# Performance work log

Measured on AMD Instinct MI355X. Metric: run time of the kernel, lower is better.

Reference implementation:

```python
import jax, jax.numpy as jnp
import numpy as np

IGNORE = 255
KA = 10.0
ITERS = 10
BETA = 0.8


def _l2(x, axis):
    # F.normalize(p=2): divide by max(norm, eps)
    return x / jnp.maximum(jnp.linalg.norm(x, axis=axis, keepdims=True), 1e-12)


def setup_inputs() -> dict:
    key = jax.random.key(0)
    k1, k2, k3, k4 = jax.random.split(key, 4)
    B, K, P, C = 8, 19, 16384, 256
    return {
        "logit": jax.random.normal(k1, (B, K, P), jnp.float32),
        "target": jax.random.randint(k2, (B, P), 0, K, jnp.int32),
        "feat": jax.random.normal(k3, (B, C, P), jnp.float32),
        "epoch": 60,
        "prototypes_dataset": _l2(jax.random.normal(k4, (C, K), jnp.float32), 0),
    }


def reference(logit, target, feat, epoch, prototypes_dataset):
    B, K, P = logit.shape
    C = feat.shape[1]
    dt = feat.dtype

    # scatter-sum per-class prototypes over all (b, p) positions; ignore bucket = K
    index = jnp.where(target == IGNORE, K, target).reshape(-1)            # [B*P]
    feat_flat = jnp.swapaxes(feat, 1, 2).reshape(B * P, C)                # [B*P, C]
    proto = jax.ops.segment_sum(feat_flat, index, num_segments=K + 1)    # [K+1, C]
    counts = jax.ops.segment_sum(jnp.ones_like(index), index, num_segments=K + 1)
    prototypes_sum = proto[:K].T                                          # [C, K]
    counts_batch = counts[:K]                                             # [K]

    # epoch is a static python int; epoch >= start_epoch(51) -> full vMF branch
    feat_norm = _l2(feat, 1)                                              # [B, C, P]
    u_init = _l2(prototypes_sum / (counts_batch.astype(dt) + 1e-6), 0)    # [C, K]
    mask0 = counts_batch == 0
    u = _l2(jnp.where(mask0[None, :], prototypes_dataset, u_init), 0)     # 'part' init
    a = jnp.full((1, 1, K), 1.0 / K, dt)

    dis = jnp.einsum('bcp,ck->bpk', feat_norm, u)                         # [B, P, K]
    e = a * jnp.exp(KA * dis)
    p = e / jnp.sum(e, -1, keepdims=True)
    for _ in range(ITERS):
        # 'avmf': second assignment in torch overwrites -> mean over batch, [1, P, K]
        a = jnp.mean(p, 0, keepdims=True)
        # 'uvmf': new prototypes from soft assignments
        u = _l2(jnp.mean(jnp.einsum('bcp,bpk->bck', feat_norm, p), 0), 0)
        dis = jnp.einsum('bcp,ck->bpk', feat_norm, u)
        e = a * jnp.exp(KA * dis)
        p = e / jnp.sum(e, -1, keepdims=True)

    # vMF_hard_loss computed in torch but 'hard' not in loss_type -> not added
    vmf_loss = jnp.mean(-p * (jnp.log(a + 1e-6) + KA * dis)) / float(np.log(K))
    consist_loss = jnp.mean(-jnp.swapaxes(p, 1, 2) * jax.nn.log_softmax(logit, axis=1))

    # contrast: off-diagonal prototype similarity over classes present in batch
    m = (~mask0).astype(dt)
    gram = u_init.T @ u_init                                              # [K, K]
    Kn = jnp.sum(m)
    contrast_loss = (jnp.sum(gram * (m[:, None] * m[None, :])) - Kn) / (Kn * (Kn - 1))

    # 'tce': truncated CE, clamp per-pixel loss at -log(beta)
    logp = jax.nn.log_softmax(logit, axis=1)                              # [B, K, P]
    safe_t = jnp.where(target == IGNORE, 0, target)
    ce = -jnp.take_along_axis(logp, safe_t[:, None, :], axis=1)[:, 0, :]  # [B, P]
    valid = (target != IGNORE).astype(dt)
    loss = jnp.sum(jnp.maximum(ce, -float(np.log(BETA))) * valid) / (jnp.sum(valid) + 1e-6)

    loss = loss + vmf_loss + contrast_loss + consist_loss
    return (loss, jax.lax.stop_gradient(prototypes_sum), jax.lax.stop_gradient(counts_batch))
```

## Files before the change

kernel.cpp:

```cpp
#include <hip/hip_runtime.h>
#include <hip/hip_bf16.h>
#include <math.h>

#define BB 8
#define KK 19
#define PP 16384
#define CC 256
#define NN (BB*PP)
#define KA_C 10.0f
#define IGNORE_L 255
#define CETHR 0.22314355131420976f
#define AQ 524288

#define OFF_FEATN   0
#define OFF_FEATNT  16777216
#define OFF_PROTO   33554432
#define OFF_COUNTS  (OFF_PROTO+4864)
#define OFF_SCAL    (OFF_COUNTS+32)
#define OFF_UINIT   (OFF_SCAL+16)
#define OFF_U       (OFF_UINIT+4864)
#define OFF_UBF     (OFF_U+4864)
#define OFF_A       (OFF_UBF+4224)
#define OFF_UPART   (OFF_A+8*AQ)
#define OFF_R1      (OFF_UPART+4980736)
#define OFF_NORM    (OFF_R1+77824)
#define OFF_LOGT    (OFF_NORM+131072)

typedef __attribute__((ext_vector_type(8))) short short8v;
typedef __attribute__((ext_vector_type(4))) float f32x4;

static __device__ __forceinline__ float bflo(unsigned int v){
    union{unsigned int i; float f;} x; x.i = v << 16; return x.f;
}
static __device__ __forceinline__ unsigned short f2bf(float f){
    union{float f; unsigned int i;} x; x.f = f;
    unsigned int r = (x.i + 0x7fffu + ((x.i >> 16) & 1u)) >> 16;
    return (unsigned short)r;
}
static __device__ __forceinline__ float rowsum16(float v){
    v += __shfl_xor(v,1); v += __shfl_xor(v,2);
    v += __shfl_xor(v,4); v += __shfl_xor(v,8);
    return v;
}
static __device__ __forceinline__ float rowmax16(float v){
    v = fmaxf(v, __shfl_xor(v,1)); v = fmaxf(v, __shfl_xor(v,2));
    v = fmaxf(v, __shfl_xor(v,4)); v = fmaxf(v, __shfl_xor(v,8));
    return v;
}

__global__ __launch_bounds__(256) void counts_kernel(const int* __restrict__ target,
                                                     float* __restrict__ ws) {
    __shared__ int cnt[KK];
    if (threadIdx.x < KK) cnt[threadIdx.x]=0;
    __syncthreads();
    for (int i = blockIdx.x*256 + threadIdx.x; i < NN; i += gridDim.x*256) {
        int t = target[i];
        if (t >= 0 && t < KK) atomicAdd(&cnt[t], 1);
    }
    __syncthreads();
    if (threadIdx.x < KK) atomicAdd(&ws[OFF_COUNTS + threadIdx.x], (float)cnt[threadIdx.x]);
}

__global__ __launch_bounds__(256) void ssct_kernel(const float* __restrict__ feat,
                                                   unsigned short* __restrict__ featn,
                                                   unsigned short* __restrict__ featn_T,
                                                   float* __restrict__ normf) {
    __shared__ float part[4][64];
    __shared__ float rn_lds[64];
    __shared__ unsigned short tTus[64][270];
    int blk = blockIdx.x;
    int b = blk >> 8;
    int px0 = (blk & 255) * 64;
    int tid = threadIdx.x;
    int l = tid & 63, w = tid >> 6;
    const float* fb = feat + (size_t)b*CC*PP;
    int c0 = w*64;
    float fv[64];
    float ss = 0.f;
#pragma unroll
    for (int cc=0; cc<64; cc++) {
        fv[cc] = fb[(size_t)(c0+cc)*PP + px0 + l];
        ss = fmaf(fv[cc], fv[cc], ss);
    }
    part[w][l] = ss;
    __syncthreads();
    if (tid < 64) {
        float s = part[0][tid]+part[1][tid]+part[2][tid]+part[3][tid];
        float nrm = fmaxf(sqrtf(s), 1e-12f);
        normf[(size_t)b*PP + px0 + tid] = nrm;
        rn_lds[tid] = 1.0f/nrm;
    }
    __syncthreads();
    float r = rn_lds[l];
    unsigned short* ob  = featn + (size_t)b*CC*PP + px0;
#pragma unroll
    for (int cc=0; cc<64; cc++) {
        int c = c0 + cc;
        unsigned short us = f2bf(fv[cc] * r);
        ob[(size_t)c*PP + l] = us;
        tTus[l][c] = us;
    }
    __syncthreads();
    unsigned short* obT = featn_T + ((size_t)b*PP + px0)*CC;
    for (int j=0; j<32; j++) {
        int flat = j*256 + tid;
        int px = flat >> 7, cu = flat & 127;
        unsigned int v = *(const unsigned int*)&tTus[px][cu*2];
        *(unsigned int*)&obT[(size_t)px*CC + cu*2] = v;
    }
}

__global__ __launch_bounds__(256) void logt_kernel(const float* __restrict__ logit,
                                                   float* __restrict__ logt) {
    __shared__ float t[256][21];
    int blk = blockIdx.x;
    int b = blk >> 6;
    int px0 = (blk & 63) * 256;
    int tid = threadIdx.x;
    for (int k=0;k<KK;k++)
        t[tid][k] = logit[((size_t)b*KK + k)*PP + px0 + tid];
    __syncthreads();
    float* dst = logt + ((size_t)b*PP + px0)*20;
    for (int j=0; j<20; j++) {
        int flat = j*256 + tid;
        int px = flat / 20, k = flat % 20;
        dst[flat] = (k<KK) ? t[px][k] : 0.f;
    }
}

__global__ __launch_bounds__(256) void proto_mfma_kernel(const unsigned short* __restrict__ featn,
                                                         const int* __restrict__ target,
                                                         const float* __restrict__ normf,
                                                         float* __restrict__ upart) {
    __shared__ int tgt_lds[4][64];
    __shared__ unsigned short nrm_lds[4][64];
    int tid = threadIdx.x;
    int blk = blockIdx.x;
    int pxtile = blk & 255;
    int bgrp = blk >> 8;
    {
        int bi = tid >> 6, j = tid & 63;
        int bb = bgrp*4 + bi;
        tgt_lds[bi][j] = target[(size_t)bb*PP + pxtile*64 + j];
        nrm_lds[bi][j] = f2bf(normf[(size_t)bb*PP + pxtile*64 + j]);
    }
    __syncthreads();
    int lane = tid & 63, wid = tid >> 6;
    int g = lane >> 4, lc = lane & 15;

    f32x4 upacc[4][2];
#pragma unroll
    for (int m=0;m<4;m++)
#pragma unroll
        for (int n=0;n<2;n++) upacc[m][n] = (f32x4){0.f,0.f,0.f,0.f};

    for (int bi=0; bi<4; bi++) {
        int bb = bgrp*4 + bi;
        union { unsigned int u[4]; short8v s; } bfr[2][2];
#pragma unroll
        for (int ks=0; ks<2; ks++) {
            int pxo = ks*32 + g*8;
#pragma unroll
            for (int j2=0;j2<4;j2++) {
                int p0i = pxo + 2*j2, p1i = pxo + 2*j2 + 1;
                int t0 = tgt_lds[bi][p0i], t1 = tgt_lds[bi][p1i];
                unsigned int n0 = nrm_lds[bi][p0i], n1 = nrm_lds[bi][p1i];
                int kk1 = lc + 16;
                bfr[ks][0].u[j2] = (t0==lc ? n0:0u) | ((t1==lc ? n1:0u)<<16);
                bfr[ks][1].u[j2] = (t0==kk1? n0:0u) | ((t1==kk1? n1:0u)<<16);
            }
        }
#pragma unroll
        for (int m=0;m<4;m++) {
            int c = wid*64 + m*16 + lc;
            const unsigned short* fr = featn + ((size_t)bb*CC + c)*PP + pxtile*64;
#pragma unroll
            for (int ks=0; ks<2; ks++) {
                int pxo = ks*32 + g*8;
                union { uint4 u4; short8v s; } af2;
                af2.u4 = *(const uint4*)&fr[pxo];
                upacc[m][0] = __builtin_amdgcn_mfma_f32_16x16x32_bf16(af2.s, bfr[ks][0].s, upacc[m][0], 0,0,0);
                upacc[m][1] = __builtin_amdgcn_mfma_f32_16x16x32_bf16(af2.s, bfr[ks][1].s, upacc[m][1], 0,0,0);
            }
        }
    }
#pragma unroll
    for (int m=0;m<4;m++) {
        int cb = wid*64 + m*16 + g*4;
#pragma unroll
        for (int n=0;n<2;n++) {
            int kk = lc + 16*n;
            if (kk < KK) {
#pragma unroll
                for (int r=0;r<4;r++)
                    upart[(size_t)blk*4864 + (size_t)(cb+r)*KK + kk] = upacc[m][n][r];
            }
        }
    }
}

__global__ __launch_bounds__(256) void setup_kernel(const float* __restrict__ pd,
                                                    float* __restrict__ ws) {
    int c = threadIdx.x;
    __shared__ float red[256];
    __shared__ float nrm[KK];
    __shared__ float lds_ui[256][KK];
    float cnts[KK], vi[KK];
#pragma unroll
    for (int k=0;k<KK;k++) cnts[k] = ws[OFF_COUNTS+k];
#pragma unroll
    for (int k=0;k<KK;k++) vi[k] = ws[OFF_PROTO + c*KK + k] / (cnts[k] + 1e-6f);
    for (int k=0;k<KK;k++) {
        red[c] = vi[k]*vi[k];
        __syncthreads();
        for (int s=128;s>0;s>>=1){ if (c<s) red[c]+=red[c+s]; __syncthreads(); }
        if (c==0) nrm[k] = fmaxf(sqrtf(red[0]), 1e-12f);
        __syncthreads();
    }
#pragma unroll
    for (int k=0;k<KK;k++) { vi[k] = vi[k]/nrm[k]; lds_ui[c][k] = vi[k]; ws[OFF_UINIT + c*KK + k] = vi[k]; }
    __syncthreads();
    float w0[KK];
#pragma unroll
    for (int k=0;k<KK;k++) w0[k] = (cnts[k]==0.f) ? pd[c*KK+k] : vi[k];
    for (int k=0;k<KK;k++) {
        red[c] = w0[k]*w0[k];
        __syncthreads();
        for (int s=128;s>0;s>>=1){ if (c<s) red[c]+=red[c+s]; __syncthreads(); }
        if (c==0) nrm[k] = fmaxf(sqrtf(red[0]), 1e-12f);
        __syncthreads();
    }
    unsigned short* ubf = (unsigned short*)(ws + OFF_UBF);
#pragma unroll
    for (int k=0;k<KK;k++) {
        float uv = w0[k] / nrm[k];
        ws[OFF_U + k*CC + c] = uv;
        ubf[k*264 + c] = f2bf(uv);
    }
    float m[KK]; float Kn=0.f;
#pragma unroll
    for (int k=0;k<KK;k++){ m[k] = (cnts[k]==0.f)?0.f:1.f; Kn += m[k]; }
    float csum = 0.f;
    for (int idx = c; idx < KK*KK; idx += 256) {
        int k1 = idx / KK, k2 = idx % KK;
        if (m[k1]!=0.f && m[k2]!=0.f) {
            float gg=0.f;
            for (int cc2=0; cc2<CC; cc2++) gg += lds_ui[cc2][k1]*lds_ui[cc2][k2];
            csum += gg;
        }
    }
    red[c]=csum; __syncthreads();
    for (int s=128;s>0;s>>=1){ if (c<s) red[c]+=red[c+s]; __syncthreads(); }
    if (c==0) ws[OFF_SCAL+4] = (red[0] - Kn) / (Kn * (Kn - 1.f));
}

__global__ __launch_bounds__(256) void pu_kernel(const unsigned short* __restrict__ featn,
                                                 const unsigned short* __restrict__ featn_T,
                                                 const unsigned short* __restrict__ ubf,
                                                 const float* __restrict__ aRbase,
                                                 float* __restrict__ aWbase,
                                                 float* __restrict__ upart,
                                                 int uniform_a) {
    __shared__ __attribute__((aligned(16))) unsigned short u_lds[32*264];
    __shared__ __attribute__((aligned(16))) unsigned short p_lds[32*72];
    int tid = threadIdx.x;
    {
        const uint4* src = (const uint4*)ubf;
        uint4* dst = (uint4*)u_lds;
        for (int i=tid; i<1056; i+=256) dst[i] = src[i];
    }
    __syncthreads();
    int blk = blockIdx.x;
    int pxtile = blk & 255;
    int bgrp = blk >> 8;
    int lane = tid & 63, wid = tid >> 6;
    int g = lane >> 4, lc = lane & 15;
    int px_w = pxtile*64 + wid*16;

    float a0r[4], a1r[4];
    if (uniform_a) {
#pragma unroll
        for (int r=0;r<4;r++){ a0r[r]=1.0f/(float)KK; a1r[r]=1.0f/(float)KK; }
    } else {
        int k1 = (lc+16 > KK-1) ? (KK-1) : (lc+16);
#pragma unroll
        for (int r=0;r<4;r++) {
            int pxg = px_w + g*4 + r;
            float s0 = aRbase[0*AQ + (size_t)pxg*32 + lc] + aRbase[1*AQ + (size_t)pxg*32 + lc]
                     + aRbase[2*AQ + (size_t)pxg*32 + lc] + aRbase[3*AQ + (size_t)pxg*32 + lc];
            float s1 = aRbase[0*AQ + (size_t)pxg*32 + k1] + aRbase[1*AQ + (size_t)pxg*32 + k1]
                     + aRbase[2*AQ + (size_t)pxg*32 + k1] + aRbase[3*AQ + (size_t)pxg*32 + k1];
            a0r[r] = s0*0.125f;
            a1r[r] = s1*0.125f;
        }
    }

    f32x4 upacc[4][2];
#pragma unroll
    for (int m=0;m<4;m++)
#pragma unroll
        for (int n=0;n<2;n++) upacc[m][n] = (f32x4){0.f,0.f,0.f,0.f};
    float aacc[2][4];
#pragma unroll
    for (int n=0;n<2;n++)
#pragma unroll
        for (int r=0;r<4;r++) aacc[n][r]=0.f;

    for (int bi=0; bi<2; bi++) {
        int bb = bgrp*2 + bi;
        const unsigned short* fb = featn + (size_t)bb*CC*PP;
        const unsigned short* fTrow = featn_T + ((size_t)bb*PP + px_w + lc)*CC;
        f32x4 acc0 = (f32x4){0.f,0.f,0.f,0.f};
        f32x4 acc1 = (f32x4){0.f,0.f,0.f,0.f};
#pragma unroll
        for (int ks=0; ks<8; ks++) {
            int cbase = ks*32 + g*8;
            union { uint4 u4; short8v s; } af, bf0, bf1;
            af.u4  = *(const uint4*)&fTrow[cbase];
            bf0.u4 = *(const uint4*)&u_lds[(size_t)lc*264 + cbase];
            bf1.u4 = *(const uint4*)&u_lds[(size_t)(lc+16)*264 + cbase];
            acc0 = __builtin_amdgcn_mfma_f32_16x16x32_bf16(af.s, bf0.s, acc0, 0,0,0);
            acc1 = __builtin_amdgcn_mfma_f32_16x16x32_bf16(af.s, bf1.s, acc1, 0,0,0);
        }
#pragma unroll
        for (int r=0;r<4;r++) {
            float e0 = a0r[r] * __expf(KA_C * acc0[r]);
            float e1 = (lc+16 < KK) ? a1r[r] * __expf(KA_C * acc1[r]) : 0.f;
            float sv = rowsum16(e0 + e1);
            float inv = 1.0f/sv;
            float p0 = e0*inv, p1 = e1*inv;
            aacc[0][r] += p0; aacc[1][r] += p1;
            int pl = wid*16 + g*4 + r;
            p_lds[(size_t)lc*72 + pl]      = f2bf(p0);
            p_lds[(size_t)(lc+16)*72 + pl] = f2bf(p1);
        }
        __syncthreads();
#pragma unroll
        for (int m=0;m<4;m++) {
            int c = wid*64 + m*16 + lc;
            const unsigned short* fr = fb + (size_t)c*PP + pxtile*64;
#pragma unroll
            for (int ks=0; ks<2; ks++) {
                int pxo = ks*32 + g*8;
                union { uint4 u4; short8v s; } af2, bp0, bp1;
                af2.u4 = *(const uint4*)&fr[pxo];
                bp0.u4 = *(const uint4*)&p_lds[(size_t)lc*72 + pxo];
                bp1.u4 = *(const uint4*)&p_lds[(size_t)(lc+16)*72 + pxo];
                upacc[m][0] = __builtin_amdgcn_mfma_f32_16x16x32_bf16(af2.s, bp0.s, upacc[m][0], 0,0,0);
                upacc[m][1] = __builtin_amdgcn_mfma_f32_16x16x32_bf16(af2.s, bp1.s, upacc[m][1], 0,0,0);
            }
        }
        __syncthreads();
    }
#pragma unroll
    for (int m=0;m<4;m++) {
        int cb = wid*64 + m*16 + g*4;
#pragma unroll
        for (int n=0;n<2;n++) {
            int kk = lc + 16*n;
            if (kk < KK) {
#pragma unroll
                for (int r=0;r<4;r++)
                    upart[(size_t)blk*4864 + (size_t)(cb+r)*KK + kk] = upacc[m][n][r];
            }
        }
    }
    float* aOut = aWbase + (size_t)bgrp*AQ;
#pragma unroll
    for (int n=0;n<2;n++) {
        int kk = lc + 16*n;
        if (kk < KK) {
#pragma unroll
            for (int r=0;r<4;r++) {
                int pxg = px_w + g*4 + r;
                aOut[(size_t)pxg*32 + kk] = aacc[n][r];
            }
        }
    }
}

__global__ __launch_bounds__(256) void r1_kernel(const float* __restrict__ upart,
                                                 float* __restrict__ r1buf) {
    int blk = blockIdx.x;
    int echunk = blk % 19;
    int ichunk = blk / 19;
    int e = echunk*256 + threadIdx.x;
    float s = 0.f;
    int i0 = ichunk*64;
    for (int i=i0; i<i0+64; i++) s += upart[(size_t)i*4864 + e];
    r1buf[(size_t)ichunk*4864 + e] = s;
}

__global__ __launch_bounds__(256) void r2_kernel(const float* __restrict__ r1buf,
                                                 float* __restrict__ ws, int nbuf) {
    int k = blockIdx.x;
    int c = threadIdx.x;
    float s = 0.f;
    for (int i=0;i<nbuf;i++) s += r1buf[(size_t)i*4864 + c*KK + k];
    __shared__ float red[256];
    red[c] = s*s; __syncthreads();
    for (int q=128;q>0;q>>=1){ if (c<q) red[c]+=red[c+q]; __syncthreads(); }
    float nrm = fmaxf(sqrtf(red[0]), 1e-12f);
    float uv = s / nrm;
    ws[OFF_U + k*CC + c] = uv;
    ((unsigned short*)(ws + OFF_UBF))[k*264 + c] = f2bf(uv);
}

__global__ __launch_bounds__(256) void protored2_kernel(const float* __restrict__ r1buf,
                                                        float* __restrict__ ws, int nbuf) {
    int e = blockIdx.x*256 + threadIdx.x;
    float s = 0.f;
    for (int i=0;i<nbuf;i++) s += r1buf[(size_t)i*4864 + e];
    ws[OFF_PROTO + e] = s;
}

__global__ __launch_bounds__(256) void final_mfma_kernel(const unsigned short* __restrict__ featn_T,
                                                         const float* __restrict__ logt,
                                                         const int* __restrict__ target,
                                                         const unsigned short* __restrict__ ubf,
                                                         const float* __restrict__ aFbase,
                                                         float* __restrict__ scal) {
    __shared__ __attribute__((aligned(16))) unsigned short u_lds[32*264];
    int tid = threadIdx.x;
    {
        const uint4* src = (const uint4*)ubf;
        uint4* dst = (uint4*)u_lds;
        for (int i=tid; i<1056; i+=256) dst[i] = src[i];
    }
    __syncthreads();
    int blk = blockIdx.x;
    int pxtile = blk & 255;
    int bgrp = blk >> 8;
    int lane = tid & 63, wid = tid >> 6;
    int g = lane >> 4, lc = lane & 15;
    int px_w = pxtile*64 + wid*16;
    bool valid1 = (lc+16) < KK;

    float v_vmf=0.f, v_cons=0.f, v_ce=0.f, v_cnt=0.f;

    for (int bi=0; bi<4; bi++) {
        int bb = bgrp*4 + bi;
        const unsigned short* fTrow = featn_T + ((size_t)bb*PP + px_w + lc)*CC;
        f32x4 acc0 = (f32x4){0.f,0.f,0.f,0.f};
        f32x4 acc1 = (f32x4){0.f,0.f,0.f,0.f};
#pragma unroll
        for (int ks=0; ks<8; ks++) {
            int cbase = ks*32 + g*8;
            union { uint4 u4; short8v s; } af, bf0, bf1;
            af.u4  = *(const uint4*)&fTrow[cbase];
            bf0.u4 = *(const uint4*)&u_lds[(size_t)lc*264 + cbase];
            bf1.u4 = *(const uint4*)&u_lds[(size_t)(lc+16)*264 + cbase];
            acc0 = __builtin_amdgcn_mfma_f32_16x16x32_bf16(af.s, bf0.s, acc0, 0,0,0);
            acc1 = __builtin_amdgcn_mfma_f32_16x16x32_bf16(af.s, bf1.s, acc1, 0,0,0);
        }
#pragma unroll
        for (int r=0;r<4;r++) {
            int pxg = px_w + g*4 + r;
            float d0 = acc0[r], d1 = acc1[r];
            float av0 = (aFbase[0*AQ + (size_t)pxg*32 + lc] + aFbase[1*AQ + (size_t)pxg*32 + lc]
                       + aFbase[2*AQ + (size_t)pxg*32 + lc] + aFbase[3*AQ + (size_t)pxg*32 + lc])*0.125f;
            float av1 = 0.f;
            if (valid1) {
                int k1 = lc+16;
                av1 = (aFbase[0*AQ + (size_t)pxg*32 + k1] + aFbase[1*AQ + (size_t)pxg*32 + k1]
                     + aFbase[2*AQ + (size_t)pxg*32 + k1] + aFbase[3*AQ + (size_t)pxg*32 + k1])*0.125f;
            }
            float e0 = av0 * __expf(KA_C * d0);
            float e1 = valid1 ? av1 * __expf(KA_C * d1) : 0.f;
            float den = rowsum16(e0 + e1);
            float inv = 1.0f/den;
            float p0 = e0*inv, p1 = e1*inv;
            float vt = -p0*(__logf(av0+1e-6f) + KA_C*d0);
            if (valid1) vt += -p1*(__logf(av1+1e-6f) + KA_C*d1);
            float vt_row = rowsum16(vt);
            const float* lrow = logt + ((size_t)bb*PP + pxg)*20;
            float lg0 = lrow[lc];
            float lg1 = valid1 ? lrow[lc+16] : -3.4e38f;
            float mx = rowmax16(fmaxf(lg0, lg1));
            float sme = __expf(lg0-mx) + (valid1 ? __expf(lg1-mx) : 0.f);
            sme = rowsum16(sme);
            float lse = mx + __logf(sme);
            float ct = -p0*(lg0-lse);
            if (valid1) ct += -p1*(lg1-lse);
            float ct_row = rowsum16(ct);
            int t = target[(size_t)bb*PP + pxg];
            float ltt = (lc==t ? lg0 : 0.f) + ((valid1 && lc+16==t) ? lg1 : 0.f);
            float lt = rowsum16(ltt);
            if (lc==0) {
                v_vmf += vt_row;
                v_cons += ct_row;
                if (t != IGNORE_L) { v_ce += fmaxf(lse - lt, CETHR); v_cnt += 1.f; }
            }
        }
    }
    __shared__ float red[4][4];
    int w = tid >> 6;
    float v0=v_vmf, v1=v_cons, v2=v_ce, v3=v_cnt;
#pragma unroll
    for (int s=32;s>0;s>>=1) {
        v0 += __shfl_xor(v0, s); v1 += __shfl_xor(v1, s);
        v2 += __shfl_xor(v2, s); v3 += __shfl_xor(v3, s);
    }
    if ((tid&63)==0){ red[w][0]=v0; red[w][1]=v1; red[w][2]=v2; red[w][3]=v3; }
    __syncthreads();
    if (tid==0) {
        atomicAdd(&scal[0], red[0][0]+red[1][0]+red[2][0]+red[3][0]);
        atomicAdd(&scal[1], red[0][1]+red[1][1]+red[2][1]+red[3][1]);
        atomicAdd(&scal[2], red[0][2]+red[1][2]+red[2][2]+red[3][2]);
        atomicAdd(&scal[3], red[0][3]+red[1][3]+red[2][3]+red[3][3]);
    }
}

__global__ __launch_bounds__(256) void finalize_kernel(const float* __restrict__ ws,
                                                       float* __restrict__ out) {
    if (blockIdx.x==0 && threadIdx.x==0) {
        float cnt_all = (float)BB*(float)PP*(float)KK;
        float vmf  = ws[OFF_SCAL+0] / cnt_all / logf((float)KK);
        float cons = ws[OFF_SCAL+1] / cnt_all;
        float ce   = ws[OFF_SCAL+2] / (ws[OFF_SCAL+3] + 1e-6f);
        float contrast = ws[OFF_SCAL+4];
        out[0] = ce + vmf + contrast + cons;
    }
    int i = blockIdx.x*256 + threadIdx.x;
    if (i < 4864) out[1+i] = ws[OFF_PROTO+i];
    if (blockIdx.x==0 && threadIdx.x < KK) out[1+4864+threadIdx.x] = ws[OFF_COUNTS+threadIdx.x];
}

extern "C" void kernel_launch(void* const* d_in, const int* in_sizes, int n_in,
                              void* d_out, int out_size, void* d_ws, size_t ws_size,
                              hipStream_t stream) {
    (void)in_sizes; (void)n_in; (void)out_size; (void)ws_size;
    const float* logit  = (const float*)d_in[0];
    const int*   target = (const int*)d_in[1];
    const float* feat   = (const float*)d_in[2];
    const float* pd     = (const float*)d_in[4];
    float* out = (float*)d_out;
    float* ws  = (float*)d_ws;

    unsigned short* featn   = (unsigned short*)ws;
    unsigned short* featn_T = (unsigned short*)(ws + OFF_FEATNT);
    unsigned short* ubf     = (unsigned short*)(ws + OFF_UBF);
    float* upart = ws + OFF_UPART;
    float* r1buf = ws + OFF_R1;
    float* normf = ws + OFF_NORM;
    float* logt  = ws + OFF_LOGT;
    float* scal  = ws + OFF_SCAL;
    float* aSet[2] = { ws + OFF_A, ws + OFF_A + (size_t)4*AQ };

    hipMemsetAsync(ws + OFF_PROTO, 0, 4912*sizeof(float), stream);
    hipMemsetAsync(ws + OFF_UBF, 0, 4224*sizeof(float), stream);
    ssct_kernel<<<2048, 256, 0, stream>>>(feat, featn, featn_T, normf);
    counts_kernel<<<256, 256, 0, stream>>>(target, ws);
    logt_kernel<<<512, 256, 0, stream>>>(logit, logt);
    proto_mfma_kernel<<<512, 256, 0, stream>>>(featn, target, normf, upart);
    r1_kernel<<<152, 256, 0, stream>>>(upart, r1buf);
    protored2_kernel<<<19, 256, 0, stream>>>(r1buf, ws, 8);
    setup_kernel<<<1, 256, 0, stream>>>(pd, ws);

    for (int t=0; t<10; t++) {
        if (t > 0) {
            r1_kernel<<<304, 256, 0, stream>>>(upart, r1buf);
            r2_kernel<<<KK, 256, 0, stream>>>(r1buf, ws, 16);
        }
        pu_kernel<<<1024, 256, 0, stream>>>(featn, featn_T, ubf,
                                            aSet[t&1], aSet[(t+1)&1],
                                            upart, (t==0)?1:0);
    }
    r1_kernel<<<304, 256, 0, stream>>>(upart, r1buf);
    r2_kernel<<<KK, 256, 0, stream>>>(r1buf, ws, 16);
    final_mfma_kernel<<<512, 256, 0, stream>>>(featn_T, logt, target, ubf, aSet[0], scal);
    finalize_kernel<<<20, 256, 0, stream>>>(ws, out);
}
```

Baseline: 594.8 us.

## Replace per-block partial buffers with atomic accumulation into 16 slots

Proto and pu kernels now atomically add their per-block prototype partials into 16 rotating slots instead of writing one full partial per block. This removes the r1 reduction kernel and its large partial buffer traffic each iteration; r2 and protored sum the 16 slots and zero them for reuse. Separately, the ssct kernel packs pairs of bf16 values via lane shuffles into 32-bit stores. The change adds atomic contention on the slots and makes the summation order nondeterministic.

```diff
diff --git a/kernel.cpp b/kernel.cpp
--- a/kernel.cpp
+++ b/kernel.cpp
@@ -22,8 +22,7 @@
 #define OFF_UBF     (OFF_U+4864)
 #define OFF_A       (OFF_UBF+4224)
 #define OFF_UPART   (OFF_A+8*AQ)
-#define OFF_R1      (OFF_UPART+4980736)
-#define OFF_NORM    (OFF_R1+77824)
+#define OFF_NORM    (OFF_UPART+77824)
 #define OFF_LOGT    (OFF_NORM+131072)
 
 typedef __attribute__((ext_vector_type(8))) short short8v;
@@ -92,13 +91,17 @@
     }
     __syncthreads();
     float r = rn_lds[l];
-    unsigned short* ob  = featn + (size_t)b*CC*PP + px0;
+    unsigned short* ob = featn + (size_t)b*CC*PP + px0;
 #pragma unroll
     for (int cc=0; cc<64; cc++) {
         int c = c0 + cc;
-        unsigned short us = f2bf(fv[cc] * r);
-        ob[(size_t)c*PP + l] = us;
-        tTus[l][c] = us;
+        unsigned int us = f2bf(fv[cc] * r);
+        tTus[l][c] = (unsigned short)us;
+        unsigned int partner = __shfl_xor(us, 1);
+        if ((l & 1) == 0) {
+            unsigned int v = us | (partner<<16);
+            *(unsigned int*)&ob[(size_t)c*PP + l] = v;
+        }
     }
     __syncthreads();
     unsigned short* obT = featn_T + ((size_t)b*PP + px0)*CC;
@@ -131,7 +134,7 @@
 __global__ __launch_bounds__(256) void proto_mfma_kernel(const unsigned short* __restrict__ featn,
                                                          const int* __restrict__ target,
                                                          const float* __restrict__ normf,
-                                                         float* __restrict__ upart) {
+                                                         float* __restrict__ up16) {
     __shared__ int tgt_lds[4][64];
     __shared__ unsigned short nrm_lds[4][64];
     int tid = threadIdx.x;
@@ -184,6 +187,7 @@
             }
         }
     }
+    float* slot = up16 + (size_t)(blk & 15)*4864;
 #pragma unroll
     for (int m=0;m<4;m++) {
         int cb = wid*64 + m*16 + g*4;
@@ -193,10 +197,21 @@
             if (kk < KK) {
 #pragma unroll
                 for (int r=0;r<4;r++)
-                    upart[(size_t)blk*4864 + (size_t)(cb+r)*KK + kk] = upacc[m][n][r];
-            }
-        }
-    }
+                    atomicAdd(&slot[(size_t)(cb+r)*KK + kk], upacc[m][n][r]);
+            }
+        }
+    }
+}
+
+__global__ __launch_bounds__(256) void protored_kernel(float* __restrict__ up16,
+                                                       float* __restrict__ ws) {
+    int e = blockIdx.x*256 + threadIdx.x;
+    float s = 0.f;
+#pragma unroll
+    for (int i=0;i<16;i++) s += up16[(size_t)i*4864 + e];
+    ws[OFF_PROTO + e] = s;
+#pragma unroll
+    for (int i=0;i<16;i++) up16[(size_t)i*4864 + e] = 0.f;
 }
 
 __global__ __launch_bounds__(256) void setup_kernel(const float* __restrict__ pd,
@@ -259,7 +274,7 @@
                                                  const unsigned short* __restrict__ ubf,
                                                  const float* __restrict__ aRbase,
                                                  float* __restrict__ aWbase,
-                                                 float* __restrict__ upart,
+                                                 float* __restrict__ up16,
                                                  int uniform_a) {
     __shared__ __attribute__((aligned(16))) unsigned short u_lds[32*264];
     __shared__ __attribute__((aligned(16))) unsigned short p_lds[32*72];
@@ -352,6 +367,7 @@
         }
         __syncthreads();
     }
+    float* slot = up16 + (size_t)(blk & 15)*4864;
 #pragma unroll
     for (int m=0;m<4;m++) {
         int cb = wid*64 + m*16 + g*4;
@@ -361,7 +377,7 @@
             if (kk < KK) {
 #pragma unroll
                 for (int r=0;r<4;r++)
-                    upart[(size_t)blk*4864 + (size_t)(cb+r)*KK + kk] = upacc[m][n][r];
+                    atomicAdd(&slot[(size_t)(cb+r)*KK + kk], upacc[m][n][r]);
             }
         }
     }
@@ -379,24 +395,13 @@
     }
 }
 
-__global__ __launch_bounds__(256) void r1_kernel(const float* __restrict__ upart,
-                                                 float* __restrict__ r1buf) {
-    int blk = blockIdx.x;
-    int echunk = blk % 19;
-    int ichunk = blk / 19;
-    int e = echunk*256 + threadIdx.x;
-    float s = 0.f;
-    int i0 = ichunk*64;
-    for (int i=i0; i<i0+64; i++) s += upart[(size_t)i*4864 + e];
-    r1buf[(size_t)ichunk*4864 + e] = s;
-}
-
-__global__ __launch_bounds__(256) void r2_kernel(const float* __restrict__ r1buf,
-                                                 float* __restrict__ ws, int nbuf) {
+__global__ __launch_bounds__(256) void r2_kernel(float* __restrict__ up16,
+                                                 float* __restrict__ ws) {
     int k = blockIdx.x;
     int c = threadIdx.x;
     float s = 0.f;
-    for (int i=0;i<nbuf;i++) s += r1buf[(size_t)i*4864 + c*KK + k];
+#pragma unroll
+    for (int i=0;i<16;i++) s += up16[(size_t)i*4864 + c*KK + k];
     __shared__ float red[256];
     red[c] = s*s; __syncthreads();
     for (int q=128;q>0;q>>=1){ if (c<q) red[c]+=red[c+q]; __syncthreads(); }
@@ -404,14 +409,8 @@
     float uv = s / nrm;
     ws[OFF_U + k*CC + c] = uv;
     ((unsigned short*)(ws + OFF_UBF))[k*264 + c] = f2bf(uv);
-}
-
-__global__ __launch_bounds__(256) void protored2_kernel(const float* __restrict__ r1buf,
-                                                        float* __restrict__ ws, int nbuf) {
-    int e = blockIdx.x*256 + threadIdx.x;
-    float s = 0.f;
-    for (int i=0;i<nbuf;i++) s += r1buf[(size_t)i*4864 + e];
-    ws[OFF_PROTO + e] = s;
+#pragma unroll
+    for (int i=0;i<16;i++) up16[(size_t)i*4864 + c*KK + k] = 0.f;
 }
 
 __global__ __launch_bounds__(256) void final_mfma_kernel(const unsigned short* __restrict__ featn_T,
@@ -540,8 +539,7 @@
     unsigned short* featn   = (unsigned short*)ws;
     unsigned short* featn_T = (unsigned short*)(ws + OFF_FEATNT);
     unsigned short* ubf     = (unsigned short*)(ws + OFF_UBF);
-    float* upart = ws + OFF_UPART;
-    float* r1buf = ws + OFF_R1;
+    float* up16  = ws + OFF_UPART;
     float* normf = ws + OFF_NORM;
     float* logt  = ws + OFF_LOGT;
     float* scal  = ws + OFF_SCAL;
@@ -549,25 +547,22 @@
 
     hipMemsetAsync(ws + OFF_PROTO, 0, 4912*sizeof(float), stream);
     hipMemsetAsync(ws + OFF_UBF, 0, 4224*sizeof(float), stream);
+    hipMemsetAsync(up16, 0, 16*4864*sizeof(float), stream);
     ssct_kernel<<<2048, 256, 0, stream>>>(feat, featn, featn_T, normf);
     counts_kernel<<<256, 256, 0, stream>>>(target, ws);
     logt_kernel<<<512, 256, 0, stream>>>(logit, logt);
-    proto_mfma_kernel<<<512, 256, 0, stream>>>(featn, target, normf, upart);
-    r1_kernel<<<152, 256, 0, stream>>>(upart, r1buf);
-    protored2_kernel<<<19, 256, 0, stream>>>(r1buf, ws, 8);
+    proto_mfma_kernel<<<512, 256, 0, stream>>>(featn, target, normf, up16);
+    protored_kernel<<<19, 256, 0, stream>>>(up16, ws);
     setup_kernel<<<1, 256, 0, stream>>>(pd, ws);
 
     for (int t=0; t<10; t++) {
-        if (t > 0) {
-            r1_kernel<<<304, 256, 0, stream>>>(upart, r1buf);
-            r2_kernel<<<KK, 256, 0, stream>>>(r1buf, ws, 16);
-        }
+        if (t > 0)
+            r2_kernel<<<KK, 256, 0, stream>>>(up16, ws);
         pu_kernel<<<1024, 256, 0, stream>>>(featn, featn_T, ubf,
                                             aSet[t&1], aSet[(t+1)&1],
-                                            upart, (t==0)?1:0);
-    }
-    r1_kernel<<<304, 256, 0, stream>>>(upart, r1buf);
-    r2_kernel<<<KK, 256, 0, stream>>>(r1buf, ws, 16);
+                                            up16, (t==0)?1:0);
+    }
+    r2_kernel<<<KK, 256, 0, stream>>>(up16, ws);
     final_mfma_kernel<<<512, 256, 0, stream>>>(featn_T, logt, target, ubf, aSet[0], scal);
     finalize_kernel<<<20, 256, 0, stream>>>(ws, out);
 }
```

After: 904.0 us. 1.52x slower.
